# Kernel optimization log

Measured on AMD Instinct MI355X. Metric: run time of the kernel, lower is better.

The kernel has to match this reference:

```python
import jax, jax.numpy as jnp
import numpy as np

EPS = 1e-6
PC_MIN = jnp.array([-50.0, -50.0, -4.0], jnp.float32)
PC_MAX = jnp.array([50.0, 50.0, 4.0], jnp.float32)
IMG_H, IMG_W = 256, 704
G, P, L, D = 1, 8, 4, 128


def _conv3x3(x, w, b):
    y = jax.lax.conv_general_dilated(x, w, (1, 1), ((1, 1), (1, 1)),
                                     dimension_numbers=('NCHW', 'OIHW', 'NCHW'))
    return y + b[None, :, None, None]


def _inorm(x):
    # InstanceNorm2d(affine=False), eps=1e-5, per-sample per-channel over (H,W)
    m = jnp.mean(x, axis=(2, 3), keepdims=True)
    v = jnp.var(x, axis=(2, 3), keepdims=True)
    return (x - m) * jax.lax.rsqrt(v + 1e-5)


def _bilinear(img, xy):
    # img: [H, W, C]; xy: [M, 2] in [0,1] (align_corners=False, zero padding)
    H, W, _ = img.shape
    px = xy[:, 0] * W - 0.5
    py = xy[:, 1] * H - 0.5
    x0 = jnp.floor(px)
    y0 = jnp.floor(py)
    wx = px - x0
    wy = py - y0
    x0 = x0.astype(jnp.int32)
    y0 = y0.astype(jnp.int32)

    def tap(xi, yi, w):
        ok = (xi >= 0) & (xi < W) & (yi >= 0) & (yi < H)
        v = img[jnp.clip(yi, 0, H - 1), jnp.clip(xi, 0, W - 1)]
        return v * (w * ok)[:, None]

    return (tap(x0, y0, (1 - wx) * (1 - wy)) + tap(x0 + 1, y0, wx * (1 - wy)) +
            tap(x0, y0 + 1, (1 - wx) * wy) + tap(x0 + 1, y0 + 1, wx * wy))


def _sampling_4d(pts, feats, scale_w, l2i):
    # pts: [B,Q,G,P,3]; feats: list of [B*G,N,Hl,Wl,C]; scale_w: [B,Q,G,1,P,L]; l2i: [B,N,4,4]
    B, Q, g, p, _ = pts.shape
    N = l2i.shape[1]
    hom = jnp.concatenate([pts, jnp.ones(pts.shape[:-1] + (1,), pts.dtype)], -1)
    cam = jnp.einsum('bnij,bqgpj->bqngpi', l2i, hom)  # project to each camera
    z = cam[..., 2:3]
    xy = cam[..., :2] / jnp.maximum(z, 1e-5)
    xy = xy / jnp.array([IMG_W, IMG_H], xy.dtype)
    xy = jnp.where(z > 1e-5, xy, -1e4)  # behind camera -> samples zero
    xy = jnp.transpose(xy, (0, 3, 2, 1, 4, 5)).reshape(B * g * N, Q * p, 2)
    out = 0.0
    for l, f in enumerate(feats):
        C = f.shape[-1]
        fi = f.reshape(B * g * N, f.shape[2], f.shape[3], C)
        s = jax.vmap(_bilinear)(fi, xy).reshape(B, g, N, Q, p, C).sum(2)  # sum over cameras
        w = jnp.transpose(scale_w[:, :, :, 0, :, l], (0, 2, 1, 3))  # [B,G,Q,P]
        out = out + s * w[..., None]
    return jnp.transpose(out, (0, 2, 1, 3, 4))  # [B,Q,G,P,C]


def _forward(feat0, feat1, feat2, feat3, lidar2img, bev_query, bev_pos,
             in_w, in_b, off_w, off_b, sw_w, sw_b,
             pe_w1, pe_b1, pe_w2, pe_b2,
             mid_w1, mid_b1, mid_w2, mid_b2, mid_w3, mid_b3,
             out_w, out_b):
    B, _, h, w = bev_query.shape
    # decoder prologue: b n (g c) H W -> (b g) n H W c  (G=1)
    feats = [jnp.transpose(f, (0, 1, 3, 4, 2)) for f in (feat0, feat1, feat2, feat3)]
    q = _inorm(bev_query + _conv3x3(bev_query, in_w, in_b))
    qf = jnp.transpose(q, (0, 2, 3, 1)).reshape(B, h * w, D)
    # sampling offsets (1x1 conv as matmul), mode='grid', scale=1.0
    off = jax.nn.sigmoid(qf @ off_w.T + off_b).reshape(B, h * w, G, P, 3)
    lim_xy = 0.25 * 1.0 + EPS
    lim_z = 4.0 + EPS
    off = jnp.concatenate([off[..., :2] * 2 * lim_xy - lim_xy,
                           off[..., 2:3] * 2 * lim_z - lim_z], -1)
    ref = bev_pos.reshape(B, h * w, 1, 1, 3) * (PC_MAX - PC_MIN) + PC_MIN
    pts = ref + off  # [B,Q,G,P,3] in world coords
    sw = (qf @ sw_w.T + sw_b).reshape(B, h * w, G, P, L)[:, :, :, None]  # b q g 1 p l
    sw = jax.nn.softmax(sw, axis=-1)
    sampled = _sampling_4d(pts, feats, sw, lidar2img)  # [B,Q,G,P,128]
    ref_n = (pts - PC_MIN) / (PC_MAX - PC_MIN)
    pe = jax.nn.relu(ref_n @ pe_w1 + pe_b1) @ pe_w2 + pe_b2  # PositionalEncodingMap MLP
    sampled = sampled + pe
    # b (h w) g p c -> b (p g c) h w
    sf = jnp.transpose(sampled, (0, 3, 2, 4, 1)).reshape(B, P * G * 128, h, w)
    m = jax.nn.gelu(jnp.einsum('oi,bihw->bohw', mid_w1, sf) + mid_b1[None, :, None, None], approximate=False)
    m = jax.nn.gelu(jnp.einsum('oi,bihw->bohw', mid_w2, m) + mid_b2[None, :, None, None], approximate=False)
    m = jnp.einsum('oi,bihw->bohw', mid_w3, m) + mid_b3[None, :, None, None]
    q = _inorm(q + m)
    q = _inorm(q + _conv3x3(q, out_w, out_b))
    height = jnp.transpose(off[..., 2], (0, 2, 3, 1)).reshape(B, G, P, h, w)
    return q, height


def _lidar2img_np():
    mats = []
    K = np.array([[500., 0., IMG_W / 2, 0.],
                  [0., 500., IMG_H / 2, 0.],
                  [0., 0., 1., 0.],
                  [0., 0., 0., 1.]])
    for n in range(6):
        th = 2 * np.pi * n / 6
        fwd = np.array([np.cos(th), np.sin(th), 0.])
        right = np.array([-np.sin(th), np.cos(th), 0.])
        down = np.array([0., 0., -1.])
        R = np.stack([right, down, fwd])
        c = fwd * 0.5 + np.array([0., 0., 1.5])
        T = np.eye(4)
        T[:3, :3] = R
        T[:3, 3] = -R @ c
        mats.append(K @ T)
    return np.stack(mats)[None].astype(np.float32)


def setup_inputs():
    key = jax.random.key(0)
    ks = jax.random.split(key, 16)

    def rn(k, shape, s=0.02):
        return jax.random.normal(k, shape, jnp.float32) * s

    B, N, h, w = 1, 6, 128, 128
    return dict(
        feat0=jax.random.normal(ks[0], (B, N, 128, 32, 88), jnp.float32),
        feat1=jax.random.normal(ks[1], (B, N, 128, 16, 44), jnp.float32),
        feat2=jax.random.normal(ks[2], (B, N, 128, 8, 22), jnp.float32),
        feat3=jax.random.normal(ks[3], (B, N, 128, 4, 11), jnp.float32),
        lidar2img=jnp.asarray(_lidar2img_np()),
        bev_query=jax.random.normal(ks[4], (B, 128, h, w), jnp.float32),
        bev_pos=jax.random.uniform(ks[5], (B, h, w, 3), jnp.float32),
        in_w=rn(ks[6], (128, 128, 3, 3)), in_b=jnp.zeros(128, jnp.float32),
        off_w=rn(ks[7], (G * P * 3, 128)),
        off_b=jax.random.uniform(ks[8], (G * P * 3,), jnp.float32, -4.0, 4.0),
        sw_w=rn(ks[9], (G * P * L, 128)), sw_b=jnp.zeros(G * P * L, jnp.float32),
        pe_w1=rn(ks[10], (3, 256), 0.5), pe_b1=jnp.zeros(256, jnp.float32),
        pe_w2=rn(ks[11], (256, 128), 0.1), pe_b2=jnp.zeros(128, jnp.float32),
        mid_w1=rn(ks[12], (512, P * 128)), mid_b1=jnp.zeros(512, jnp.float32),
        mid_w2=rn(ks[13], (512, 512)), mid_b2=jnp.zeros(512, jnp.float32),
        mid_w3=rn(ks[14], (128, 512)), mid_b3=jnp.zeros(128, jnp.float32),
        out_w=rn(ks[15], (128, 128, 3, 3)), out_b=jnp.zeros(128, jnp.float32),
    )


def reference(feat0, feat1, feat2, feat3, lidar2img, bev_query, bev_pos,
              in_w, in_b, off_w, off_b, sw_w, sw_b,
              pe_w1, pe_b1, pe_w2, pe_b2,
              mid_w1, mid_b1, mid_w2, mid_b2, mid_w3, mid_b3,
              out_w, out_b):
    return _forward(feat0, feat1, feat2, feat3, lidar2img, bev_query, bev_pos,
                    in_w, in_b, off_w, off_b, sw_w, sw_b,
                    pe_w1, pe_b1, pe_w2, pe_b2,
                    mid_w1, mid_b1, mid_w2, mid_b2, mid_w3, mid_b3,
                    out_w, out_b)
```

## Files before the change

### kernel.cpp

```cpp
#include <hip/hip_runtime.h>
#include <hip/hip_bf16.h>
#include <math.h>

#define HW 16384

typedef __attribute__((ext_vector_type(8))) short short8;
typedef __attribute__((ext_vector_type(4))) float floatx4;
typedef __attribute__((ext_vector_type(2))) float floatx2;

__device__ __forceinline__ float gelu_exact(float x){
    return 0.5f * x * (1.0f + erff(x * 0.7071067811865475f));
}

__device__ __forceinline__ floatx2 bf2x(unsigned int u){
    floatx2 r;
    r.x = __uint_as_float(u << 16);
    r.y = __uint_as_float(u & 0xffff0000u);
    return r;
}

__global__ __launch_bounds__(256) void feat_transpose_all_k(
    const float* __restrict__ f0, const float* __restrict__ f1,
    const float* __restrict__ f2, const float* __restrict__ f3,
    __hip_bfloat16* __restrict__ out)
{
    int idx = blockIdx.x * 256 + threadIdx.x;
    const float* in; int Hl, Wl, base;
    if (idx < 2162688)      { in = f0; Hl = 32; Wl = 88; base = 0; }
    else if (idx < 2703360) { in = f1; Hl = 16; Wl = 44; base = 2162688; }
    else if (idx < 2838528) { in = f2; Hl = 8;  Wl = 22; base = 2703360; }
    else                    { in = f3; Hl = 4;  Wl = 11; base = 2838528; }
    int r   = idx - base;
    int c   = r & 127;
    int pix = r >> 7;
    int x   = pix % Wl;
    int tt  = pix / Wl;
    int y   = tt % Hl;
    int n   = tt / Hl;
    out[idx] = __float2bfloat16(in[((n * 128 + c) * Hl + y) * Wl + x]);
}

__global__ __launch_bounds__(256) void prep_k(
    const float* __restrict__ mid_w1, const float* __restrict__ mid_w2,
    const float* __restrict__ mid_w3, const float* __restrict__ pe_w2,
    const float* __restrict__ off_w,  const float* __restrict__ off_b,
    const float* __restrict__ sw_w,   const float* __restrict__ sw_b,
    const float* __restrict__ in_w,   const float* __restrict__ out_w,
    __hip_bfloat16* __restrict__ Wb1, __hip_bfloat16* __restrict__ Wb2,
    __hip_bfloat16* __restrict__ Wb3, __hip_bfloat16* __restrict__ Wpe,
    __hip_bfloat16* __restrict__ Wof, float* __restrict__ Bof,
    __hip_bfloat16* __restrict__ Wcv1, __hip_bfloat16* __restrict__ Wcv2)
{
    int b = blockIdx.x, t = threadIdx.x;
    if (b < 2048) {
        int i = b * 256 + t; Wb1[i] = __float2bfloat16(mid_w1[i]);
    } else if (b < 3072) {
        int i = (b - 2048) * 256 + t; Wb2[i] = __float2bfloat16(mid_w2[i]);
    } else if (b < 3328) {
        int i = (b - 3072) * 256 + t; Wb3[i] = __float2bfloat16(mid_w3[i]);
    } else if (b < 3456) {
        int n = b - 3328; Wpe[n * 256 + t] = __float2bfloat16(pe_w2[t * 128 + n]);
    } else if (b < 3584) {
        int n = b - 3456;
        if (t < 128) {
            float w = 0.f;
            if (n < 24)      w = off_w[n * 128 + t];
            else if (n < 56) w = sw_w[(n - 24) * 128 + t];
            Wof[n * 128 + t] = __float2bfloat16(w);
            if (t == 0) Bof[n] = (n < 24) ? off_b[n] : ((n < 56) ? sw_b[n - 24] : 0.f);
        }
    } else if (b < 3712) {
        int o = b - 3584;
        for (int idx = t; idx < 1152; idx += 256) {
            int s = idx >> 7, i = idx & 127;
            Wcv1[o * 1152 + idx] = __float2bfloat16(in_w[(o * 128 + i) * 9 + s]);
        }
    } else {
        int o = b - 3712;
        for (int idx = t; idx < 1152; idx += 256) {
            int s = idx >> 7, i = idx & 127;
            Wcv2[o * 1152 + idx] = __float2bfloat16(out_w[(o * 128 + i) * 9 + s]);
        }
    }
}

__global__ __launch_bounds__(256) void chw2hwc_pad_k(
    const float* __restrict__ q, const float* __restrict__ stats,
    __hip_bfloat16* __restrict__ out)
{
    __shared__ float tile[128][65];
    __shared__ float sm[128], sr[128];
    int t = threadIdx.x;
    if (t < 128) {
        if (stats) {
            float s = stats[2 * t], s2 = stats[2 * t + 1];
            float mean = s * (1.0f / HW);
            sm[t] = mean;
            sr[t] = rsqrtf(s2 * (1.0f / HW) - mean * mean + 1e-5f);
        } else {
            sm[t] = 0.f; sr[t] = 1.f;
        }
    }
    int b = blockIdx.x;
    int y = b >> 1, x0 = (b & 1) * 64;
    int xi = t & 63, c0 = t >> 6;
    for (int c = c0; c < 128; c += 4)
        tile[c][xi] = q[c * HW + y * 128 + x0 + xi];
    __syncthreads();
    int xp = t >> 2, cg = (t & 3) * 32;
    __hip_bfloat16* dst = out + ((size_t)(y + 1) * 130 + (x0 + 1 + xp)) * 128;
    #pragma unroll
    for (int g = 0; g < 4; g++) {
        int c = cg + g * 8;
        union { __hip_bfloat16 h[8]; uint4 u; } pk;
        #pragma unroll
        for (int j = 0; j < 8; j++)
            pk.h[j] = __float2bfloat16((tile[c + j][xp] - sm[c + j]) * sr[c + j]);
        *(uint4*)&dst[c] = pk.u;
    }
}

template<int BM, int BN, int ACT, int OUTT, int CONV>
__global__ __launch_bounds__(256) void bgemm_k(
    const __hip_bfloat16* __restrict__ X, const __hip_bfloat16* __restrict__ W,
    const float* __restrict__ bias, void* __restrict__ outp,
    const float* __restrict__ res,
    const float* __restrict__ rstats, float* __restrict__ ostats,
    int M, int K, int N)
{
    constexpr int ROWS = BM + BN;
    __shared__ __align__(16) __hip_bfloat16 SH[ROWS * 32];
    __hip_bfloat16* As = SH;
    __hip_bfloat16* Bs = SH + BM * 32;
    int t = threadIdx.x;
    int w = t >> 6, lane = t & 63;
    int mb = blockIdx.y * BM, nb = blockIdx.x * BN;
    int cy = mb >> 7, cx = mb & 127;
    constexpr int WM = BM / 2;
    constexpr int MI = WM / 16;
    constexpr int NJ = BN / 32;
    int wm = (w & 1) * WM, wn = (w >> 1) * (BN / 2);
    int lm = lane & 15, lq = lane >> 4;
    floatx4 zero = {0.f, 0.f, 0.f, 0.f};
    floatx4 acc[MI][NJ];
    #pragma unroll
    for (int i = 0; i < MI; i++)
        #pragma unroll
        for (int j = 0; j < NJ; j++) acc[i][j] = zero;
    constexpr int ITERS = (ROWS * 4) / 256;
    for (int kb = 0; kb < K; kb += 32) {
        int s = kb >> 7;
        int dyi = s / 3, dxi = s - dyi * 3;
        __syncthreads();
        #pragma unroll
        for (int it = 0; it < ITERS; it++) {
            int chunk = it * 256 + t;
            int row = chunk >> 2, ko = (chunk & 3) * 8;
            const __hip_bfloat16* src;
            if (row < BM) {
                if (CONV)
                    src = X + (((size_t)(cy + dyi) * 130) + (cx + dxi + row)) * 128 + (kb & 127) + ko;
                else
                    src = X + (size_t)(mb + row) * K + kb + ko;
            } else {
                src = W + (size_t)(nb + row - BM) * K + kb + ko;
            }
            __builtin_amdgcn_global_load_lds(
                (const __attribute__((address_space(1))) void*)src,
                (__attribute__((address_space(3))) void*)&SH[(size_t)(it * 256 + (t & ~63)) * 8],
                16, 0, 0);
        }
        __syncthreads();
        short8 af[MI], bf[NJ];
        #pragma unroll
        for (int i = 0; i < MI; i++)
            af[i] = *(const short8*)&As[(wm + i * 16 + lm) * 32 + lq * 8];
        #pragma unroll
        for (int j = 0; j < NJ; j++)
            bf[j] = *(const short8*)&Bs[(wn + j * 16 + lm) * 32 + lq * 8];
        #pragma unroll
        for (int i = 0; i < MI; i++)
            #pragma unroll
            for (int j = 0; j < NJ; j++)
                acc[i][j] = __builtin_amdgcn_mfma_f32_16x16x32_bf16(af[i], bf[j], acc[i][j], 0, 0, 0);
    }
    float invM = 1.0f / (float)M;
    #pragma unroll
    for (int j = 0; j < NJ; j++) {
        int n = nb + wn + j * 16 + lm;
        float bv = bias[n];
        float rmean = 0.f, rrstd = 0.f;
        if (OUTT == 1 && res && rstats) {
            float s = rstats[2 * n], s2 = rstats[2 * n + 1];
            rmean = s * invM;
            rrstd = rsqrtf(s2 * invM - rmean * rmean + 1e-5f);
        }
        float ss = 0.f, ss2 = 0.f;
        #pragma unroll
        for (int i = 0; i < MI; i++) {
            #pragma unroll
            for (int r = 0; r < 4; r++) {
                int m = mb + wm + i * 16 + lq * 4 + r;
                float v = acc[i][j][r] + bv;
                if (ACT) v = gelu_exact(v);
                if (OUTT == 0) {
                    ((__hip_bfloat16*)outp)[(size_t)m * N + n] = __float2bfloat16(v);
                } else {
                    if (res) {
                        float rv = res[(size_t)n * M + m];
                        v += rstats ? (rv - rmean) * rrstd : rv;
                    }
                    ((float*)outp)[(size_t)n * M + m] = v;
                    ss += v; ss2 += v * v;
                }
            }
        }
        if (OUTT == 1 && ostats) {
            ss  += __shfl_xor(ss, 16);  ss  += __shfl_xor(ss, 32);
            ss2 += __shfl_xor(ss2, 16); ss2 += __shfl_xor(ss2, 32);
            if (lq == 0) {
                atomicAdd(&ostats[2 * n], ss);
                atomicAdd(&ostats[2 * n + 1], ss2);
            }
        }
    }
}

__global__ __launch_bounds__(256) void pe_bgemm_k(
    const float* __restrict__ pts, const float* __restrict__ pe_w1,
    const float* __restrict__ pe_b1, const __hip_bfloat16* __restrict__ W,
    const float* __restrict__ bias, __hip_bfloat16* __restrict__ out)
{
    __shared__ __align__(16) __hip_bfloat16 As[128 * 32];
    __shared__ __align__(16) __hip_bfloat16 Bs[128 * 32];
    __shared__ __align__(16) float wps[4][256];
    int t = threadIdx.x;
    int w = t >> 6, lane = t & 63;
    int mb = blockIdx.x * 128;
    {
        int d = t >> 6, c = (t & 63) * 4;
        float4 v;
        if (d == 0) v = *(const float4*)&pe_b1[c];
        else        v = *(const float4*)&pe_w1[(d - 1) * 256 + c];
        *(float4*)&wps[d][c] = v;
    }
    int cg = t & 3;
    int r0 = t >> 2;
    float rn[2][3];
    #pragma unroll
    for (int h = 0; h < 2; h++) {
        int r = mb + r0 + h * 64;
        rn[h][0] = (pts[(size_t)r * 3 + 0] + 50.f) * 0.01f;
        rn[h][1] = (pts[(size_t)r * 3 + 1] + 50.f) * 0.01f;
        rn[h][2] = (pts[(size_t)r * 3 + 2] + 4.f) * 0.125f;
    }
    int wm = (w & 1) * 64, wn = (w >> 1) * 64;
    int lm = lane & 15, lq = lane >> 4;
    floatx4 zero = {0.f, 0.f, 0.f, 0.f};
    floatx4 acc[4][4];
    #pragma unroll
    for (int i = 0; i < 4; i++)
        #pragma unroll
        for (int j = 0; j < 4; j++) acc[i][j] = zero;
    for (int kb = 0; kb < 256; kb += 32) {
        __syncthreads();
        #pragma unroll
        for (int it = 0; it < 2; it++) {
            int chunk = it * 256 + t;
            int brow = chunk >> 2, ko = (chunk & 3) * 8;
            const __hip_bfloat16* src = W + (size_t)brow * 256 + kb + ko;
            __builtin_amdgcn_global_load_lds(
                (const __attribute__((address_space(1))) void*)src,
                (__attribute__((address_space(3))) void*)&Bs[(size_t)(it * 256 + (t & ~63)) * 8],
                16, 0, 0);
        }
        int c0 = kb + cg * 8;
        float4 bva = *(const float4*)&wps[0][c0], bvb = *(const float4*)&wps[0][c0 + 4];
        float4 wxa = *(const float4*)&wps[1][c0], wxb = *(const float4*)&wps[1][c0 + 4];
        float4 wya = *(const float4*)&wps[2][c0], wyb = *(const float4*)&wps[2][c0 + 4];
        float4 wza = *(const float4*)&wps[3][c0], wzb = *(const float4*)&wps[3][c0 + 4];
        #pragma unroll
        for (int h = 0; h < 2; h++) {
            const float* bv = (const float*)&bva;
            const float* wx = (const float*)&wxa;
            const float* wy = (const float*)&wya;
            const float* wz = (const float*)&wza;
            union { __hip_bfloat16 hh[8]; uint4 u; } pk;
            #pragma unroll
            for (int j = 0; j < 4; j++) {
                float v = bv[j] + rn[h][0] * wx[j] + rn[h][1] * wy[j] + rn[h][2] * wz[j];
                pk.hh[j] = __float2bfloat16(fmaxf(v, 0.f));
            }
            bv = (const float*)&bvb; wx = (const float*)&wxb;
            wy = (const float*)&wyb; wz = (const float*)&wzb;
            #pragma unroll
            for (int j = 0; j < 4; j++) {
                float v = bv[j] + rn[h][0] * wx[j] + rn[h][1] * wy[j] + rn[h][2] * wz[j];
                pk.hh[4 + j] = __float2bfloat16(fmaxf(v, 0.f));
            }
            *(uint4*)&As[(r0 + h * 64) * 32 + cg * 8] = pk.u;
        }
        __syncthreads();
        short8 af[4], bf[4];
        #pragma unroll
        for (int i = 0; i < 4; i++)
            af[i] = *(const short8*)&As[(wm + i * 16 + lm) * 32 + lq * 8];
        #pragma unroll
        for (int j = 0; j < 4; j++)
            bf[j] = *(const short8*)&Bs[(wn + j * 16 + lm) * 32 + lq * 8];
        #pragma unroll
        for (int i = 0; i < 4; i++)
            #pragma unroll
            for (int j = 0; j < 4; j++)
                acc[i][j] = __builtin_amdgcn_mfma_f32_16x16x32_bf16(af[i], bf[j], acc[i][j], 0, 0, 0);
    }
    #pragma unroll
    for (int i = 0; i < 4; i++) {
        #pragma unroll
        for (int j = 0; j < 4; j++) {
            int n = wn + j * 16 + lm;
            float bv = bias[n];
            #pragma unroll
            for (int r = 0; r < 4; r++) {
                int m = mb + wm + i * 16 + lq * 4 + r;
                out[(size_t)m * 128 + n] = __float2bfloat16(acc[i][j][r] + bv);
            }
        }
    }
}

__global__ __launch_bounds__(256) void inorm_apply_k(
    const float* __restrict__ in, const float* __restrict__ stats, float* __restrict__ out)
{
    int b = blockIdx.x;
    int c = b >> 3, seg = b & 7;
    float s = stats[2 * c], s2 = stats[2 * c + 1];
    float mean = s * (1.0f / HW);
    float rstd = rsqrtf(s2 * (1.0f / HW) - mean * mean + 1e-5f);
    const float4* pi = (const float4*)(in + (size_t)c * HW + seg * 2048);
    float4*       po = (float4*)(out + (size_t)c * HW + seg * 2048);
    int t = threadIdx.x;
    #pragma unroll
    for (int k = 0; k < 2; k++) {
        float4 v = pi[t + k * 256];
        v.x = (v.x - mean) * rstd; v.y = (v.y - mean) * rstd;
        v.z = (v.z - mean) * rstd; v.w = (v.w - mean) * rstd;
        po[t + k * 256] = v;
    }
}

__global__ __launch_bounds__(256) void offpost_k(
    const float* __restrict__ raw, const float* __restrict__ bev_pos,
    float* __restrict__ pts, float* __restrict__ swn, float* __restrict__ height_out)
{
    int pix = blockIdx.x * 256 + threadIdx.x;
    const float pcmin[3] = {-50.f, -50.f, -4.f};
    const float rng[3]   = {100.f, 100.f, 8.f};
    float bp[3];
    #pragma unroll
    for (int d = 0; d < 3; d++) bp[d] = bev_pos[pix * 3 + d];
    #pragma unroll
    for (int p = 0; p < 8; p++) {
        #pragma unroll
        for (int d = 0; d < 3; d++) {
            float acc = raw[(p * 3 + d) * HW + pix];
            float sv = 1.f / (1.f + expf(-acc));
            float lim = (d == 2) ? (4.0f + 1e-6f) : (0.25f + 1e-6f);
            float offv = sv * 2.f * lim - lim;
            float refv = bp[d] * rng[d] + pcmin[d];
            pts[pix * 24 + p * 3 + d] = refv + offv;
            if (d == 2) height_out[p * HW + pix] = offv;
        }
        float r[4], m = -1e30f;
        #pragma unroll
        for (int l = 0; l < 4; l++) {
            r[l] = raw[(24 + p * 4 + l) * HW + pix];
            m = fmaxf(m, r[l]);
        }
        float sum = 0.f;
        #pragma unroll
        for (int l = 0; l < 4; l++) { r[l] = expf(r[l] - m); sum += r[l]; }
        float inv = 1.f / sum;
        #pragma unroll
        for (int l = 0; l < 4; l++) swn[pix * 32 + p * 4 + l] = r[l] * inv;
    }
}

__global__ __launch_bounds__(256) void sample_k(
    const __hip_bfloat16* __restrict__ featT, const float* __restrict__ pts,
    const float* __restrict__ swn,   const float* __restrict__ l2i,
    __hip_bfloat16* __restrict__ sf)
{
    int pix = blockIdx.x;
    int t = threadIdx.x;
    int lane = t & 63, wv = t >> 6;
    __shared__ float pts_s[24];
    __shared__ float swl_s[32];
    __shared__ float M[96];
    __shared__ __align__(16) int   offs[8][24][4];
    __shared__ __align__(16) float wts[8][24][4];
    __shared__ int cnt[8];
    if (t < 96) M[t] = l2i[t];
    if (t < 24) pts_s[t] = pts[pix * 24 + t];
    if (t < 32) swl_s[t] = swn[pix * 32 + t];
    if (t < 8)  cnt[t] = 0;
    __syncthreads();

    floatx2 acc[2];
    #pragma unroll
    for (int i = 0; i < 2; i++) {
        unsigned int u = *(const unsigned int*)&sf[(size_t)pix * 1024 + (wv * 2 + i) * 128 + 2 * lane];
        acc[i] = bf2x(u);
    }

    const int lHt[4] = {32, 16, 8, 4}, lWt[4] = {88, 44, 22, 11};
    const int loff[4] = {0, 2162688, 2703360, 2838528};
    if (t < 192) {
        int p = t / 24;
        int rr = t - p * 24;
        int n = rr >> 2, l = rr & 3;
        float X = pts_s[p * 3], Y = pts_s[p * 3 + 1], Z = pts_s[p * 3 + 2];
        const float* Mn = &M[n * 16];
        float zc = Mn[8] * X + Mn[9] * Y + Mn[10] * Z + Mn[11];
        if (zc > 1e-5f) {
            float inv = 1.f / zc;
            float xn = (Mn[0] * X + Mn[1] * Y + Mn[2] * Z + Mn[3]) * inv * (1.f / 704.f);
            float yn = (Mn[4] * X + Mn[5] * Y + Mn[6] * Z + Mn[7]) * inv * (1.f / 256.f);
            int Wl = lWt[l], Hl = lHt[l];
            float px = xn * Wl - 0.5f, py = yn * Hl - 0.5f;
            px = fminf(fmaxf(px, -2.f), (float)(Wl + 1));
            py = fminf(fmaxf(py, -2.f), (float)(Hl + 1));
            float x0f = floorf(px), y0f = floorf(py);
            float wx = px - x0f, wy = py - y0f;
            int x0 = (int)x0f, y0 = (int)y0f;
            bool xi0 = (unsigned)x0 < (unsigned)Wl, xi1 = (unsigned)(x0 + 1) < (unsigned)Wl;
            bool yi0 = (unsigned)y0 < (unsigned)Hl, yi1 = (unsigned)(y0 + 1) < (unsigned)Hl;
            if ((xi0 || xi1) && (yi0 || yi1)) {
                float wl = swl_s[p * 4 + l];
                float w00 = wl * (1.f - wx) * (1.f - wy) * (float)(xi0 && yi0);
                float w10 = wl * wx * (1.f - wy)         * (float)(xi1 && yi0);
                float w01 = wl * (1.f - wx) * wy         * (float)(xi0 && yi1);
                float w11 = wl * wx * wy                 * (float)(xi1 && yi1);
                int x0c = min(max(x0, 0), Wl - 1), x1c = min(max(x0 + 1, 0), Wl - 1);
                int y0c = min(max(y0, 0), Hl - 1), y1c = min(max(y0 + 1, 0), Hl - 1);
                int base = loff[l] + n * Hl * Wl * 128;
                int idx = atomicAdd(&cnt[p], 1);
                offs[p][idx][0] = (base + (y0c * Wl + x0c) * 128) * 2;
                offs[p][idx][1] = (base + (y0c * Wl + x1c) * 128) * 2;
                offs[p][idx][2] = (base + (y1c * Wl + x0c) * 128) * 2;
                offs[p][idx][3] = (base + (y1c * Wl + x1c) * 128) * 2;
                wts[p][idx][0] = w00; wts[p][idx][1] = w10;
                wts[p][idx][2] = w01; wts[p][idx][3] = w11;
            }
        }
    }
    __syncthreads();

    const char* fbase = (const char*)featT;
    int lane4 = lane * 4;
    #pragma unroll
    for (int i = 0; i < 2; i++) {
        int p = wv * 2 + i;
        int np = cnt[p];
        floatx2 a0 = acc[i];
        floatx2 a1 = {0.f, 0.f};
        int j = 0;
        #pragma unroll 1
        for (; j + 2 <= np; j += 2) {
            int4   oA = *(const int4*)&offs[p][j][0];
            float4 wA = *(const float4*)&wts[p][j][0];
            int4   oB = *(const int4*)&offs[p][j + 1][0];
            float4 wB = *(const float4*)&wts[p][j + 1][0];
            unsigned int v0 = *(const unsigned int*)(fbase + (unsigned)(oA.x + lane4));
            unsigned int v1 = *(const unsigned int*)(fbase + (unsigned)(oA.y + lane4));
            unsigned int v2 = *(const unsigned int*)(fbase + (unsigned)(oA.z + lane4));
            unsigned int v3 = *(const unsigned int*)(fbase + (unsigned)(oA.w + lane4));
            unsigned int v4 = *(const unsigned int*)(fbase + (unsigned)(oB.x + lane4));
            unsigned int v5 = *(const unsigned int*)(fbase + (unsigned)(oB.y + lane4));
            unsigned int v6 = *(const unsigned int*)(fbase + (unsigned)(oB.z + lane4));
            unsigned int v7 = *(const unsigned int*)(fbase + (unsigned)(oB.w + lane4));
            a0 += bf2x(v0) * wA.x;
            a0 += bf2x(v1) * wA.y;
            a0 += bf2x(v2) * wA.z;
            a0 += bf2x(v3) * wA.w;
            a1 += bf2x(v4) * wB.x;
            a1 += bf2x(v5) * wB.y;
            a1 += bf2x(v6) * wB.z;
            a1 += bf2x(v7) * wB.w;
        }
        if (j < np) {
            int4   o = *(const int4*)&offs[p][j][0];
            float4 w = *(const float4*)&wts[p][j][0];
            unsigned int v0 = *(const unsigned int*)(fbase + (unsigned)(o.x + lane4));
            unsigned int v1 = *(const unsigned int*)(fbase + (unsigned)(o.y + lane4));
            unsigned int v2 = *(const unsigned int*)(fbase + (unsigned)(o.z + lane4));
            unsigned int v3 = *(const unsigned int*)(fbase + (unsigned)(o.w + lane4));
            a0 += bf2x(v0) * w.x;
            a0 += bf2x(v1) * w.y;
            a0 += bf2x(v2) * w.z;
            a0 += bf2x(v3) * w.w;
        }
        acc[i] = a0 + a1;
    }
    #pragma unroll
    for (int i = 0; i < 2; i++) {
        union { __hip_bfloat16 h[2]; unsigned int u; } pk;
        pk.h[0] = __float2bfloat16(acc[i].x);
        pk.h[1] = __float2bfloat16(acc[i].y);
        *(unsigned int*)&sf[(size_t)pix * 1024 + (wv * 2 + i) * 128 + 2 * lane] = pk.u;
    }
}

extern "C" void kernel_launch(void* const* d_in, const int* in_sizes, int n_in,
                              void* d_out, int out_size, void* d_ws, size_t ws_size,
                              hipStream_t stream)
{
    const float* feat[4] = {(const float*)d_in[0], (const float*)d_in[1],
                            (const float*)d_in[2], (const float*)d_in[3]};
    const float* l2i       = (const float*)d_in[4];
    const float* bev_query = (const float*)d_in[5];
    const float* bev_pos   = (const float*)d_in[6];
    const float* in_w  = (const float*)d_in[7];  const float* in_b  = (const float*)d_in[8];
    const float* off_w = (const float*)d_in[9];  const float* off_b = (const float*)d_in[10];
    const float* sw_w  = (const float*)d_in[11]; const float* sw_b  = (const float*)d_in[12];
    const float* pe_w1 = (const float*)d_in[13]; const float* pe_b1 = (const float*)d_in[14];
    const float* pe_w2 = (const float*)d_in[15]; const float* pe_b2 = (const float*)d_in[16];
    const float* mid_w1 = (const float*)d_in[17]; const float* mid_b1 = (const float*)d_in[18];
    const float* mid_w2 = (const float*)d_in[19]; const float* mid_b2 = (const float*)d_in[20];
    const float* mid_w3 = (const float*)d_in[21]; const float* mid_b3 = (const float*)d_in[22];
    const float* out_w  = (const float*)d_in[23]; const float* out_b  = (const float*)d_in[24];

    float* ws = (float*)d_ws;
    float* fTf = ws;
    __hip_bfloat16* fT = (__hip_bfloat16*)fTf;
    float* Bb  = fTf + 1436160;
    float* Cb  = Bb + 2097152;
    float* Gb  = Cb + 2097152;
    float* Dp  = Gb + 2097152;
    float* Eb  = Dp + 393216;
    float* QTf = Eb + 524288;
    __hip_bfloat16* qT = (__hip_bfloat16*)QTf;
    float* SFf = QTf + 1081600;
    __hip_bfloat16* sfb = (__hip_bfloat16*)SFf;
    float* M1f = SFf + 8388608;
    __hip_bfloat16* m1b = (__hip_bfloat16*)M1f;
    float* M2f = M1f + 4194304;
    __hip_bfloat16* m2b = (__hip_bfloat16*)M2f;
    float* WC1 = M2f + 4194304;
    __hip_bfloat16* Wcv1 = (__hip_bfloat16*)WC1;
    float* WC2 = WC1 + 73728;
    __hip_bfloat16* Wcv2 = (__hip_bfloat16*)WC2;
    float* W1f = WC2 + 73728;
    __hip_bfloat16* Wb1 = (__hip_bfloat16*)W1f;
    float* W2f = W1f + 262144;
    __hip_bfloat16* Wb2 = (__hip_bfloat16*)W2f;
    float* W3f = W2f + 131072;
    __hip_bfloat16* Wb3 = (__hip_bfloat16*)W3f;
    float* WPf = W3f + 32768;
    __hip_bfloat16* Wpe = (__hip_bfloat16*)WPf;
    float* WOf = WPf + 16384;
    __hip_bfloat16* Wof = (__hip_bfloat16*)WOf;
    float* Bof = WOf + 8192;
    float* Stats = Bof + 128;
    float* stats1 = Stats;
    float* stats2 = Stats + 256;
    float* stats3 = Stats + 512;

    float* q_out = (float*)d_out;
    float* h_out = q_out + 2097152;

    hipMemsetAsync(qT, 0, (size_t)130 * 130 * 128 * sizeof(__hip_bfloat16), stream);
    hipMemsetAsync(Stats, 0, 768 * sizeof(float), stream);

    feat_transpose_all_k<<<11220, 256, 0, stream>>>(feat[0], feat[1], feat[2], feat[3], fT);
    prep_k<<<3840, 256, 0, stream>>>(mid_w1, mid_w2, mid_w3, pe_w2, off_w, off_b, sw_w, sw_b,
                                     in_w, out_w, Wb1, Wb2, Wb3, Wpe, Wof, Bof, Wcv1, Wcv2);

    chw2hwc_pad_k<<<256, 256, 0, stream>>>(bev_query, nullptr, qT);
    bgemm_k<64, 64, 0, 1, 1><<<dim3(2, 256), 256, 0, stream>>>(
        qT, Wcv1, in_b, Cb, bev_query, nullptr, stats1, HW, 1152, 128);

    chw2hwc_pad_k<<<256, 256, 0, stream>>>(Cb, stats1, qT);
    bgemm_k<64, 64, 0, 1, 1><<<dim3(2, 256), 256, 0, stream>>>(
        qT + 131 * 128, Wof, Bof, Bb, nullptr, nullptr, nullptr, HW, 128, 128);
    offpost_k<<<64, 256, 0, stream>>>(Bb, bev_pos, Dp, Eb, h_out);

    pe_bgemm_k<<<1024, 256, 0, stream>>>(Dp, pe_w1, pe_b1, Wpe, pe_b2, sfb);

    sample_k<<<HW, 256, 0, stream>>>(fT, Dp, Eb, l2i, sfb);

    bgemm_k<128, 128, 1, 0, 0><<<dim3(4, 128), 256, 0, stream>>>(
        sfb, Wb1, mid_b1, m1b, nullptr, nullptr, nullptr, HW, 1024, 512);
    bgemm_k<128, 128, 1, 0, 0><<<dim3(4, 128), 256, 0, stream>>>(
        m1b, Wb2, mid_b2, m2b, nullptr, nullptr, nullptr, HW, 512, 512);
    bgemm_k<64, 64, 0, 1, 0><<<dim3(2, 256), 256, 0, stream>>>(
        m2b, Wb3, mid_b3, Bb, Cb, stats1, stats2, HW, 512, 128);

    chw2hwc_pad_k<<<256, 256, 0, stream>>>(Bb, stats2, qT);
    bgemm_k<64, 64, 0, 1, 1><<<dim3(2, 256), 256, 0, stream>>>(
        qT, Wcv2, out_b, Gb, Bb, stats2, stats3, HW, 1152, 128);
    inorm_apply_k<<<1024, 256, 0, stream>>>(Gb, stats3, q_out);
}
```

Baseline: 427.7 us.

## Multi-buffer GEMM LDS staging with async prefetch and XOR swizzle

Replaces the single-buffer load/sync/compute loop in the bf16 MFMA GEMM with a 3- or 4-stage ring of LDS buffers. Global-to-LDS loads for future k-steps are issued ahead of time, gated by manual vmcnt waits and one barrier per step. It also XOR-swizzles the 16-byte chunk positions within each row to reduce LDS bank conflicts on fragment reads. The cost is more shared memory per block, which may lower occupancy, and the hand-coded vmcnt counts depend on the exact number of outstanding loads.

```diff
diff --git a/kernel.cpp b/kernel.cpp
--- a/kernel.cpp
+++ b/kernel.cpp
@@ -129,9 +129,10 @@
     int M, int K, int N)
 {
     constexpr int ROWS = BM + BN;
-    __shared__ __align__(16) __hip_bfloat16 SH[ROWS * 32];
-    __hip_bfloat16* As = SH;
-    __hip_bfloat16* Bs = SH + BM * 32;
+    constexpr int ITERS = (ROWS * 4) / 256;
+    constexpr int BUFE  = ROWS * 32;
+    constexpr int NBUF  = (ITERS == 2) ? 4 : 3;
+    __shared__ __align__(16) __hip_bfloat16 SH[NBUF * BUFE];
     int t = threadIdx.x;
     int w = t >> 6, lane = t & 63;
     int mb = blockIdx.y * BM, nb = blockIdx.x * BN;
@@ -141,49 +142,75 @@
     constexpr int NJ = BN / 32;
     int wm = (w & 1) * WM, wn = (w >> 1) * (BN / 2);
     int lm = lane & 15, lq = lane >> 4;
+    int sl = (lq ^ ((lm >> 1) & 3)) * 8;
     floatx4 zero = {0.f, 0.f, 0.f, 0.f};
     floatx4 acc[MI][NJ];
     #pragma unroll
     for (int i = 0; i < MI; i++)
         #pragma unroll
         for (int j = 0; j < NJ; j++) acc[i][j] = zero;
-    constexpr int ITERS = (ROWS * 4) / 256;
-    for (int kb = 0; kb < K; kb += 32) {
-        int s = kb >> 7;
-        int dyi = s / 3, dxi = s - dyi * 3;
-        __syncthreads();
+
+    const int nsteps = K >> 5;
+
+    auto STAGE = [&](int bufi, int tk2) {
+        int kb_ = tk2 * 32;
+        int s_ = kb_ >> 7;
+        int dyi_ = s_ / 3, dxi_ = s_ - dyi_ * 3;
         #pragma unroll
         for (int it = 0; it < ITERS; it++) {
             int chunk = it * 256 + t;
-            int row = chunk >> 2, ko = (chunk & 3) * 8;
+            int row = chunk >> 2;
+            int ko = ((chunk & 3) ^ ((row >> 1) & 3)) * 8;
             const __hip_bfloat16* src;
             if (row < BM) {
                 if (CONV)
-                    src = X + (((size_t)(cy + dyi) * 130) + (cx + dxi + row)) * 128 + (kb & 127) + ko;
+                    src = X + (((size_t)(cy + dyi_) * 130) + (cx + dxi_ + row)) * 128 + (kb_ & 127) + ko;
                 else
-                    src = X + (size_t)(mb + row) * K + kb + ko;
+                    src = X + (size_t)(mb + row) * K + kb_ + ko;
             } else {
-                src = W + (size_t)(nb + row - BM) * K + kb + ko;
+                src = W + (size_t)(nb + row - BM) * K + kb_ + ko;
             }
             __builtin_amdgcn_global_load_lds(
                 (const __attribute__((address_space(1))) void*)src,
-                (__attribute__((address_space(3))) void*)&SH[(size_t)(it * 256 + (t & ~63)) * 8],
+                (__attribute__((address_space(3))) void*)&SH[bufi * BUFE + (it * 256 + (t & ~63)) * 8],
                 16, 0, 0);
         }
-        __syncthreads();
+    };
+
+    #pragma unroll
+    for (int pi = 0; pi < NBUF - 1; pi++)
+        if (pi < nsteps) STAGE(pi, pi);
+
+    for (int tk = 0; tk < nsteps; ++tk) {
+        int rem = nsteps - 1 - tk;
+        if constexpr (ITERS == 2) {
+            if (rem >= 2)      asm volatile("s_waitcnt vmcnt(4)" ::: "memory");
+            else if (rem == 1) asm volatile("s_waitcnt vmcnt(2)" ::: "memory");
+            else               asm volatile("s_waitcnt vmcnt(0)" ::: "memory");
+        } else {
+            if (rem >= 1)      asm volatile("s_waitcnt vmcnt(4)" ::: "memory");
+            else               asm volatile("s_waitcnt vmcnt(0)" ::: "memory");
+        }
+        __builtin_amdgcn_s_barrier();
+        int tkn = tk + NBUF - 1;
+        if (tkn < nsteps) STAGE(tkn % NBUF, tkn);
+
+        const __hip_bfloat16* As = SH + (tk % NBUF) * BUFE;
+        const __hip_bfloat16* Bs = As + BM * 32;
         short8 af[MI], bf[NJ];
         #pragma unroll
         for (int i = 0; i < MI; i++)
-            af[i] = *(const short8*)&As[(wm + i * 16 + lm) * 32 + lq * 8];
+            af[i] = *(const short8*)&As[(wm + i * 16 + lm) * 32 + sl];
         #pragma unroll
         for (int j = 0; j < NJ; j++)
-            bf[j] = *(const short8*)&Bs[(wn + j * 16 + lm) * 32 + lq * 8];
+            bf[j] = *(const short8*)&Bs[(wn + j * 16 + lm) * 32 + sl];
         #pragma unroll
         for (int i = 0; i < MI; i++)
             #pragma unroll
             for (int j = 0; j < NJ; j++)
                 acc[i][j] = __builtin_amdgcn_mfma_f32_16x16x32_bf16(af[i], bf[j], acc[i][j], 0, 0, 0);
     }
+
     float invM = 1.0f / (float)M;
     #pragma unroll
     for (int j = 0; j < NJ; j++) {
```

After: 395.4 us. 1.08x faster.
